# Performance work log

Measured on AMD Instinct MI355X. Metric: run time of the kernel, lower is better.

Reference implementation:

```python
import jax, jax.numpy as jnp
import numpy as np

SEQ, BATCH, IN_DIM, HID, NQ = 256, 512, 512, 512, 32


def setup_inputs() -> dict:
    key = jax.random.key(0)
    k_in, k_fw, k_fb, k_ow, k_ob = jax.random.split(key, 5)
    s_fc = 1.0 / np.sqrt(IN_DIM + HID)
    s_out = 1.0 / np.sqrt(NQ)
    return {
        "inputs": jax.random.normal(k_in, (SEQ, BATCH, IN_DIM), dtype=jnp.float32),
        "fc_w": jax.random.uniform(k_fw, (NQ, IN_DIM + HID), jnp.float32, -s_fc, s_fc),
        "fc_b": jax.random.uniform(k_fb, (NQ,), jnp.float32, -s_fc, s_fc),
        "out_w": jax.random.uniform(k_ow, (HID, NQ), jnp.float32, -s_out, s_out),
        "out_b": jax.random.uniform(k_ob, (HID,), jnp.float32, -s_out, s_out),
    }


def _quantum_gate(q_in):
    # RX(x_i) on wire i then CNOT ladder; <Z_k> = prod_{j<=k} cos(x_j)
    return jnp.cumprod(jnp.cos(q_in), axis=-1)


def reference(inputs, fc_w, fc_b, out_w, out_b):
    batch = inputs.shape[1]
    h0 = jnp.zeros((batch, HID), dtype=inputs.dtype)
    c0 = jnp.zeros((batch, HID), dtype=inputs.dtype)

    def step(carry, x):
        hx, cx = carry
        combined = jnp.concatenate([x, hx], axis=1)            # [B, IN+HID]
        q_in = combined @ fc_w.T + fc_b                        # [B, NQ]
        q = _quantum_gate(q_in)                                # [B, NQ]
        f = jax.nn.sigmoid(q) @ out_w.T + out_b                # [B, HID]
        i = f                                                  # same circuit & weights as f
        g = jnp.tanh(q) @ out_w.T + out_b
        o = f                                                  # same as f
        cx = f * cx + i * g
        hx = o * jnp.tanh(cx)
        return (hx, cx), hx

    (hx, cx), outputs = jax.lax.scan(step, (h0, c0), inputs)
    return outputs, hx, cx
```

## Files before the change

kernel.cpp:

```cpp
#include <hip/hip_runtime.h>
#include <math.h>

#define SEQ 256
#define BATCH 512
#define IN_DIM 512
#define HID 512
#define NQ 32

typedef float v2f __attribute__((ext_vector_type(2)));

__device__ __forceinline__ float fast_rcp(float x) { return __builtin_amdgcn_rcpf(x); }

__device__ __forceinline__ float tanh_fast(float x) {
    float a = fabsf(x);
    float e = __expf(-2.0f * a);
    float r = (1.0f - e) * fast_rcp(1.0f + e);
    return copysignf(r, x);
}

template <int CTRL>
__device__ __forceinline__ float dpp_add(float x) {
    int t = __builtin_amdgcn_update_dpp(0, __float_as_int(x), CTRL, 0xF, 0xF, false);
    return x + __int_as_float(t);
}
__device__ __forceinline__ float reduce16_add(float x) {
    x = dpp_add<0xB1>(x);
    x = dpp_add<0x4E>(x);
    x = dpp_add<0x141>(x);
    x = dpp_add<0x140>(x);
    return x;
}
template <int CTRL, int ROW_MASK>
__device__ __forceinline__ float dpp_mul1(float x) {
    int t = __builtin_amdgcn_update_dpp(0x3f800000 , __float_as_int(x),
                                        CTRL, ROW_MASK, 0xF, false);
    return x * __int_as_float(t);
}
__device__ __forceinline__ float scan32_mul(float x) {
    x = dpp_mul1<0x111, 0xF>(x);
    x = dpp_mul1<0x112, 0xF>(x);
    x = dpp_mul1<0x114, 0xF>(x);
    x = dpp_mul1<0x118, 0xF>(x);
    x = dpp_mul1<0x142, 0xA>(x);
    return x;
}

#define BLOCK_BARRIER_LDS() asm volatile("s_waitcnt lgkmcnt(0)\n\ts_barrier" ::: "memory")

__global__ __launch_bounds__(256, 4) void xp_kernel(const float* __restrict__ x,
                                                    const float* __restrict__ fc_w,
                                                    const float* __restrict__ fc_b,
                                                    float* __restrict__ xp) {
    const int tid = threadIdx.x;
    const int g2 = tid >> 4;
    const int s  = tid & 15;

    __shared__ float4 tile4[16 * 128];

    v2f wA_lo[8], wA_hi[8], wB_lo[8], wB_hi[8];
    {
        const float* wrA = fc_w + (size_t)(g2 * 2 + 0) * (IN_DIM + HID) + 4 * s;
        const float* wrB = fc_w + (size_t)(g2 * 2 + 1) * (IN_DIM + HID) + 4 * s;
#pragma unroll
        for (int j = 0; j < 8; ++j) {
            float4 a = *reinterpret_cast<const float4*>(wrA + 64 * j);
            float4 b = *reinterpret_cast<const float4*>(wrB + 64 * j);
            wA_lo[j] = (v2f){a.x, a.y}; wA_hi[j] = (v2f){a.z, a.w};
            wB_lo[j] = (v2f){b.x, b.y}; wB_hi[j] = (v2f){b.z, b.w};
        }
    }
    const float2 bias2 = reinterpret_cast<const float2*>(fc_b)[g2];

    const float4* x4 = reinterpret_cast<const float4*>(x) + (size_t)blockIdx.x * (16 * 128);
#pragma unroll
    for (int q = 0; q < 8; ++q)
        tile4[tid + 256 * q] = x4[tid + 256 * q];
    __syncthreads();

    const int row0 = blockIdx.x * 16;
    float2* xp2 = reinterpret_cast<float2*>(xp);
    for (int rp = 0; rp < 8; ++rp) {
        const int r0 = 2 * rp, r1 = 2 * rp + 1;
        v2f aA0 = (v2f){0.f, 0.f}, aA1 = aA0, aB0 = aA0, aB1 = aA0;
        v2f bA0 = aA0, bA1 = aA0, bB0 = aA0, bB1 = aA0;
#pragma unroll
        for (int j = 0; j < 8; j += 2) {
            float4 h0 = tile4[r0 * 128 + s + 16 * j];
            float4 h1 = tile4[r1 * 128 + s + 16 * j];
            v2f h0lo = (v2f){h0.x, h0.y}, h0hi = (v2f){h0.z, h0.w};
            v2f h1lo = (v2f){h1.x, h1.y}, h1hi = (v2f){h1.z, h1.w};
            aA0 = __builtin_elementwise_fma(h0lo, wA_lo[j], aA0);
            aA0 = __builtin_elementwise_fma(h0hi, wA_hi[j], aA0);
            aA1 = __builtin_elementwise_fma(h0lo, wB_lo[j], aA1);
            aA1 = __builtin_elementwise_fma(h0hi, wB_hi[j], aA1);
            aB0 = __builtin_elementwise_fma(h1lo, wA_lo[j], aB0);
            aB0 = __builtin_elementwise_fma(h1hi, wA_hi[j], aB0);
            aB1 = __builtin_elementwise_fma(h1lo, wB_lo[j], aB1);
            aB1 = __builtin_elementwise_fma(h1hi, wB_hi[j], aB1);
            float4 g0 = tile4[r0 * 128 + s + 16 * (j + 1)];
            float4 g1 = tile4[r1 * 128 + s + 16 * (j + 1)];
            v2f g0lo = (v2f){g0.x, g0.y}, g0hi = (v2f){g0.z, g0.w};
            v2f g1lo = (v2f){g1.x, g1.y}, g1hi = (v2f){g1.z, g1.w};
            bA0 = __builtin_elementwise_fma(g0lo, wA_lo[j + 1], bA0);
            bA0 = __builtin_elementwise_fma(g0hi, wA_hi[j + 1], bA0);
            bA1 = __builtin_elementwise_fma(g0lo, wB_lo[j + 1], bA1);
            bA1 = __builtin_elementwise_fma(g0hi, wB_hi[j + 1], bA1);
            bB0 = __builtin_elementwise_fma(g1lo, wA_lo[j + 1], bB0);
            bB0 = __builtin_elementwise_fma(g1hi, wA_hi[j + 1], bB0);
            bB1 = __builtin_elementwise_fma(g1lo, wB_lo[j + 1], bB1);
            bB1 = __builtin_elementwise_fma(g1hi, wB_hi[j + 1], bB1);
        }
        v2f sA0 = aA0 + bA0, sA1 = aA1 + bA1, sB0 = aB0 + bB0, sB1 = aB1 + bB1;
        float rA0 = reduce16_add(sA0.x + sA0.y);
        float rA1 = reduce16_add(sA1.x + sA1.y);
        float rB0 = reduce16_add(sB0.x + sB0.y);
        float rB1 = reduce16_add(sB1.x + sB1.y);
        if (s == 0) {
            xp2[(size_t)(row0 + r0) * 16 + g2] = make_float2(rA0 + bias2.x, rA1 + bias2.y);
            xp2[(size_t)(row0 + r1) * 16 + g2] = make_float2(rB0 + bias2.x, rB1 + bias2.y);
        }
    }
}

__global__ __launch_bounds__(512)
__attribute__((amdgpu_waves_per_eu(4, 4)))
void rnn_kernel(const float* __restrict__ xp,
                const float* __restrict__ fc_w,
                const float* __restrict__ out_w,
                const float* __restrict__ out_b,
                float* __restrict__ out) {
    const int b = blockIdx.x;
    const int tid = threadIdx.x;
    const int w8 = tid >> 6;
    const int lane = tid & 63;
    const int l31 = lane & 31;
    const int grp = lane >> 1;
    const int sl = lane & 1;

    __shared__ __align__(16) float hbuf[HID];
    __shared__ __align__(16) float pbuf[2][8][NQ];
    __shared__ __align__(16) float pwbuf[8][64];
    __shared__ __align__(16) float xps[SEQ * NQ];

    v2f wh_lo[8], wh_hi[8];
    {
        const float* wr = fc_w + (size_t)grp * (IN_DIM + HID) + IN_DIM + 64 * w8 + 4 * sl;
#pragma unroll
        for (int j = 0; j < 8; ++j) {
            float4 a = *reinterpret_cast<const float4*>(wr + 8 * j);
            wh_lo[j] = (v2f){a.x, a.y}; wh_hi[j] = (v2f){a.z, a.w};
        }
    }
    const int hid = 64 * w8 + lane;
    v2f owv[16];
    {
        const float4* o = reinterpret_cast<const float4*>(out_w + (size_t)hid * NQ);
#pragma unroll
        for (int q4 = 0; q4 < 8; ++q4) {
            float4 a = o[q4];
            owv[2 * q4 + 0] = (v2f){a.x, a.y};
            owv[2 * q4 + 1] = (v2f){a.z, a.w};
        }
    }
    const float ob = out_b[hid];

    {
        const float4* xpg = reinterpret_cast<const float4*>(xp);
        float4* xps4 = reinterpret_cast<float4*>(xps);
#pragma unroll
        for (int k = 0; k < 4; ++k) {
            int idx = tid + 512 * k;
            int t = idx >> 3, q4 = idx & 7;
            xps4[idx] = xpg[((size_t)t * BATCH + b) * 8 + q4];
        }
    }
    hbuf[tid] = 0.0f;
    float c = 0.0f;
    __syncthreads();

    float* hx_out = out + (size_t)SEQ * BATCH * HID + (size_t)b * HID;
    float* cx_out = hx_out + (size_t)BATCH * HID;

    const float4* h4s = reinterpret_cast<const float4*>(hbuf) + (16 * w8 + sl);

    int par = 0;
    for (int t = 0; t < SEQ; ++t) {
        v2f aA = (v2f){0.f, 0.f}, bA = aA;
#pragma unroll
        for (int j = 0; j < 8; j += 2) {
            float4 hv = h4s[2 * j];
            aA = __builtin_elementwise_fma((v2f){hv.x, hv.y}, wh_lo[j], aA);
            aA = __builtin_elementwise_fma((v2f){hv.z, hv.w}, wh_hi[j], aA);
            float4 gv = h4s[2 * (j + 1)];
            bA = __builtin_elementwise_fma((v2f){gv.x, gv.y}, wh_lo[j + 1], bA);
            bA = __builtin_elementwise_fma((v2f){gv.z, gv.w}, wh_hi[j + 1], bA);
        }
        v2f sA = aA + bA;
        float r = dpp_add<0xB1>(sA.x + sA.y);
        if (sl == 0) pbuf[par][w8][grp] = r;

        BLOCK_BARRIER_LDS();

        {
            const float* pb = &pbuf[par][0][0];
            float q01 = pb[l31] + pb[32 + l31];
            float q23 = pb[64 + l31] + pb[96 + l31];
            float q45 = pb[128 + l31] + pb[160 + l31];
            float q67 = pb[192 + l31] + pb[224 + l31];
            float qin = ((q01 + q23) + (q45 + q67)) + xps[t * NQ + l31];
            float pp = scan32_mul(__cosf(qin));
            float arg = (lane < 32) ? -pp : (-2.0f * pp);
            float e = __expf(arg);
            float num = (lane < 32) ? 1.0f : (1.0f - e);
            float val = num * fast_rcp(1.0f + e);
            pwbuf[w8][lane] = val;
        }

        const float4* sb4 = reinterpret_cast<const float4*>(&pwbuf[w8][0]);
        const float4* tb4 = sb4 + 8;
        v2f fa = (v2f){0.f, 0.f}, fb = fa, ga = fa, gb = fa;
#pragma unroll
        for (int m = 0; m < 8; ++m) {
            float4 sv = sb4[m];
            float4 tv = tb4[m];
            fa = __builtin_elementwise_fma((v2f){sv.x, sv.y}, owv[2 * m + 0], fa);
            fb = __builtin_elementwise_fma((v2f){sv.z, sv.w}, owv[2 * m + 1], fb);
            ga = __builtin_elementwise_fma((v2f){tv.x, tv.y}, owv[2 * m + 0], ga);
            gb = __builtin_elementwise_fma((v2f){tv.z, tv.w}, owv[2 * m + 1], gb);
        }
        v2f sf = fa + fb, sg = ga + gb;
        float f = ob + sf.x + sf.y;
        float g = ob + sg.x + sg.y;
        c = f * (c + g);
        float h = f * tanh_fast(c);

        hbuf[hid] = h;
        out[((size_t)t * BATCH + b) * HID + hid] = h;
        if (t == SEQ - 1) {
            hx_out[hid] = h;
            cx_out[hid] = c;
        }
        par ^= 1;
    }
}

extern "C" void kernel_launch(void* const* d_in, const int* in_sizes, int n_in,
                              void* d_out, int out_size, void* d_ws, size_t ws_size,
                              hipStream_t stream) {
    const float* inputs = (const float*)d_in[0];
    const float* fc_w   = (const float*)d_in[1];
    const float* fc_b   = (const float*)d_in[2];
    const float* out_w  = (const float*)d_in[3];
    const float* out_b  = (const float*)d_in[4];
    float* out = (float*)d_out;
    float* xp  = (float*)d_ws;

    xp_kernel<<<(SEQ * BATCH) / 16, 256, 0, stream>>>(inputs, fc_w, fc_b, xp);
    rnn_kernel<<<BATCH, 512, 0, stream>>>(xp, fc_w, out_w, out_b, out);
}
```

Before: 408.5 us.

## Process two batch rows per block with interleaved software-pipelined phases

```diff
diff --git a/kernel.cpp b/kernel.cpp
--- a/kernel.cpp
+++ b/kernel.cpp
@@ -123,24 +123,24 @@
 }
 
 __global__ __launch_bounds__(512)
-__attribute__((amdgpu_waves_per_eu(4, 4)))
+__attribute__((amdgpu_waves_per_eu(2, 2)))
 void rnn_kernel(const float* __restrict__ xp,
                 const float* __restrict__ fc_w,
                 const float* __restrict__ out_w,
                 const float* __restrict__ out_b,
                 float* __restrict__ out) {
-    const int b = blockIdx.x;
     const int tid = threadIdx.x;
     const int w8 = tid >> 6;
     const int lane = tid & 63;
     const int l31 = lane & 31;
     const int grp = lane >> 1;
     const int sl = lane & 1;
-
-    __shared__ __align__(16) float hbuf[HID];
-    __shared__ __align__(16) float pbuf[2][8][NQ];
-    __shared__ __align__(16) float pwbuf[8][64];
-    __shared__ __align__(16) float xps[SEQ * NQ];
+    const int bb[2] = {2 * (int)blockIdx.x, 2 * (int)blockIdx.x + 1};
+
+    __shared__ __align__(16) float hbuf[2][HID];
+    __shared__ __align__(16) float pbuf[2][2][8][NQ];
+    __shared__ __align__(16) float pwbuf[2][8][64];
+    __shared__ __align__(16) float xps[2][SEQ * NQ];
 
     v2f wh_lo[8], wh_hi[8];
     {
@@ -166,57 +166,58 @@
 
     {
         const float4* xpg = reinterpret_cast<const float4*>(xp);
-        float4* xps4 = reinterpret_cast<float4*>(xps);
-#pragma unroll
-        for (int k = 0; k < 4; ++k) {
-            int idx = tid + 512 * k;
-            int t = idx >> 3, q4 = idx & 7;
-            xps4[idx] = xpg[((size_t)t * BATCH + b) * 8 + q4];
-        }
-    }
-    hbuf[tid] = 0.0f;
-    float c = 0.0f;
+#pragma unroll
+        for (int bi = 0; bi < 2; ++bi) {
+            float4* xps4 = reinterpret_cast<float4*>(&xps[bi][0]);
+#pragma unroll
+            for (int k = 0; k < 4; ++k) {
+                int idx = tid + 512 * k;
+                int t = idx >> 3, q4 = idx & 7;
+                xps4[idx] = xpg[((size_t)t * BATCH + bb[bi]) * 8 + q4];
+            }
+        }
+    }
+    hbuf[0][tid & 511] = 0.0f;
+    hbuf[1][tid & 511] = 0.0f;
+    float c0 = 0.0f, c1 = 0.0f;
     __syncthreads();
 
-    float* hx_out = out + (size_t)SEQ * BATCH * HID + (size_t)b * HID;
+    float* hx_out = out + (size_t)SEQ * BATCH * HID;
     float* cx_out = hx_out + (size_t)BATCH * HID;
 
-    const float4* h4s = reinterpret_cast<const float4*>(hbuf) + (16 * w8 + sl);
-
-    int par = 0;
-    for (int t = 0; t < SEQ; ++t) {
+    auto phaseA = [&](int bi, int tt, int pw) {
+        (void)tt;
+        const float4* h4 = reinterpret_cast<const float4*>(&hbuf[bi][0]) + (16 * w8 + sl);
         v2f aA = (v2f){0.f, 0.f}, bA = aA;
 #pragma unroll
         for (int j = 0; j < 8; j += 2) {
-            float4 hv = h4s[2 * j];
+            float4 hv = h4[2 * j];
             aA = __builtin_elementwise_fma((v2f){hv.x, hv.y}, wh_lo[j], aA);
             aA = __builtin_elementwise_fma((v2f){hv.z, hv.w}, wh_hi[j], aA);
-            float4 gv = h4s[2 * (j + 1)];
+            float4 gv = h4[2 * j + 2];
             bA = __builtin_elementwise_fma((v2f){gv.x, gv.y}, wh_lo[j + 1], bA);
             bA = __builtin_elementwise_fma((v2f){gv.z, gv.w}, wh_hi[j + 1], bA);
         }
         v2f sA = aA + bA;
         float r = dpp_add<0xB1>(sA.x + sA.y);
-        if (sl == 0) pbuf[par][w8][grp] = r;
-
-        BLOCK_BARRIER_LDS();
-
-        {
-            const float* pb = &pbuf[par][0][0];
-            float q01 = pb[l31] + pb[32 + l31];
-            float q23 = pb[64 + l31] + pb[96 + l31];
-            float q45 = pb[128 + l31] + pb[160 + l31];
-            float q67 = pb[192 + l31] + pb[224 + l31];
-            float qin = ((q01 + q23) + (q45 + q67)) + xps[t * NQ + l31];
-            float pp = scan32_mul(__cosf(qin));
-            float arg = (lane < 32) ? -pp : (-2.0f * pp);
-            float e = __expf(arg);
-            float num = (lane < 32) ? 1.0f : (1.0f - e);
-            float val = num * fast_rcp(1.0f + e);
-            pwbuf[w8][lane] = val;
-        }
-
-        const float4* sb4 = reinterpret_cast<const float4*>(&pwbuf[w8][0]);
+        if (sl == 0) pbuf[bi][pw][w8][grp] = r;
+    };
+    auto phaseB = [&](int bi, int pr, int tt) {
+        const float* pb = &pbuf[bi][pr][0][0];
+        float q01 = pb[l31] + pb[32 + l31];
+        float q23 = pb[64 + l31] + pb[96 + l31];
+        float q45 = pb[128 + l31] + pb[160 + l31];
+        float q67 = pb[192 + l31] + pb[224 + l31];
+        float qin = ((q01 + q23) + (q45 + q67)) + xps[bi][tt * NQ + l31];
+        float pp = scan32_mul(__cosf(qin));
+        float arg = (lane < 32) ? -pp : (-2.0f * pp);
+        float e = __expf(arg);
+        float num = (lane < 32) ? 1.0f : (1.0f - e);
+        float val = num * fast_rcp(1.0f + e);
+        pwbuf[bi][w8][lane] = val;
+    };
+    auto phaseC = [&](int bi, int tt, float& c) {
+        const float4* sb4 = reinterpret_cast<const float4*>(&pwbuf[bi][w8][0]);
         const float4* tb4 = sb4 + 8;
         v2f fa = (v2f){0.f, 0.f}, fb = fa, ga = fa, gb = fa;
 #pragma unroll
@@ -233,14 +234,33 @@
         float g = ob + sg.x + sg.y;
         c = f * (c + g);
         float h = f * tanh_fast(c);
-
-        hbuf[hid] = h;
-        out[((size_t)t * BATCH + b) * HID + hid] = h;
-        if (t == SEQ - 1) {
-            hx_out[hid] = h;
-            cx_out[hid] = c;
-        }
-        par ^= 1;
+        hbuf[bi][hid] = h;
+        out[((size_t)tt * BATCH + bb[bi]) * HID + hid] = h;
+        if (tt == SEQ - 1) {
+            hx_out[(size_t)bb[bi] * HID + hid] = h;
+            cx_out[(size_t)bb[bi] * HID + hid] = c;
+        }
+    };
+
+    int p0 = 0, p1 = 0;
+    phaseA(0, 0, p0);
+    BLOCK_BARRIER_LDS();
+    phaseB(0, p0, 0);
+    phaseA(1, 0, p1);
+    phaseC(0, 0, c0);
+    BLOCK_BARRIER_LDS();
+
+    for (int t = 0; t < SEQ; ++t) {
+        phaseB(1, p1, t);
+        if (t + 1 < SEQ) { p0 ^= 1; phaseA(0, t + 1, p0); }
+        phaseC(1, t, c1);
+        BLOCK_BARRIER_LDS();
+        if (t + 1 < SEQ) {
+            phaseB(0, p0, t + 1);
+            p1 ^= 1; phaseA(1, t + 1, p1);
+            phaseC(0, t + 1, c0);
+            BLOCK_BARRIER_LDS();
+        }
     }
 }
 
@@ -256,5 +276,5 @@
     float* xp  = (float*)d_ws;
 
     xp_kernel<<<(SEQ * BATCH) / 16, 256, 0, stream>>>(inputs, fc_w, fc_b, xp);
-    rnn_kernel<<<BATCH, 512, 0, stream>>>(xp, fc_w, out_w, out_b, out);
-}
+    rnn_kernel<<<BATCH / 2, 512, 0, stream>>>(xp, fc_w, out_w, out_b, out);
+}
```

New measurement: 467.9 us. 1.15x slower.
